# Optimization experiments

Hardware: AMD Instinct MI355X
Metric: run time of the kernel (lower is better)

Reference implementation:

```python
import jax, jax.numpy as jnp
import numpy as np

NUM_HEADS = 16
DIM_HEAD = 64
HIDDEN = 1024
CONTEXT = 200
MAX_POS = 512
INNER = NUM_HEADS * DIM_HEAD


def setup_inputs() -> dict:
    key = jax.random.key(0)
    ks = jax.random.split(key, 8)
    B, T = 8, 4000  # T is a multiple of CONTEXT (remainder == 0)
    s = 0.02
    return {
        "hidden_states": jax.random.normal(ks[0], (B, T, HIDDEN), jnp.float32),
        "ln_w": jnp.ones((HIDDEN,), jnp.float32),
        "ln_b": jnp.zeros((HIDDEN,), jnp.float32),
        "wq": jax.random.normal(ks[1], (HIDDEN, INNER), jnp.float32) * s,
        "wkv": jax.random.normal(ks[2], (HIDDEN, 2 * INNER), jnp.float32) * s,
        "wo": jax.random.normal(ks[3], (INNER, HIDDEN), jnp.float32) * s,
        "bo": jnp.zeros((HIDDEN,), jnp.float32),
        "rel_emb": jax.random.normal(ks[4], (2 * MAX_POS + 1, DIM_HEAD), jnp.float32) * s,
    }


def reference(hidden_states, ln_w, ln_b, wq, wkv, wo, bo, rel_emb):
    B, T, _ = hidden_states.shape
    nb = T // CONTEXT  # remainder == 0 by construction
    scale = DIM_HEAD ** -0.5

    # pre-norm (LayerNorm, eps=1e-5)
    mu = jnp.mean(hidden_states, axis=-1, keepdims=True)
    var = jnp.mean(jnp.square(hidden_states - mu), axis=-1, keepdims=True)
    x = (hidden_states - mu) * jax.lax.rsqrt(var + 1e-5) * ln_w + ln_b

    q = x @ wq                       # (B, T, INNER)
    kv = x @ wkv                     # (B, T, 2*INNER)
    k, v = jnp.split(kv, 2, axis=-1)

    def blk(t):  # (B, T, INNER) -> (B, nb, H, C, D)
        return t.reshape(B, nb, CONTEXT, NUM_HEADS, DIM_HEAD).transpose(0, 1, 3, 2, 4)

    q, k, v = blk(q), blk(k), blk(v)

    # Shaw relative position embeddings within a block
    seq = jnp.arange(CONTEXT)
    dist = jnp.clip(seq[:, None] - seq[None, :], -CONTEXT, CONTEXT) + MAX_POS
    rel = rel_emb[dist]              # (C, C, D)

    # pos bias: sum over head dim of q * rel  (einsum instead of broadcast-multiply-sum)
    pos_attn = jnp.einsum('bnhid,ijd->bnhij', q, rel) * scale

    # SDPA math path: softmax(q k^T * scale + bias) v
    scores = jnp.einsum('bnhid,bnhjd->bnhij', q, k) * scale + pos_attn
    attn = jax.nn.softmax(scores, axis=-1)
    out = jnp.einsum('bnhij,bnhjd->bnhid', attn, v)  # (B, nb, H, C, D)

    out = out.transpose(0, 1, 3, 2, 4).reshape(B, T, INNER)
    return out @ wo + bo  # dropout is identity in eval
```

## Files before the change

kernel.cpp:

```cpp
#include <hip/hip_runtime.h>
#include <stdint.h>
#include <stddef.h>

#define NTOK   32000
#define HID    1024
#define NQKV   3072
#define CTX    200
#define NH     16

typedef _Float16 f16;
typedef _Float16 f16x8 __attribute__((ext_vector_type(8)));
typedef _Float16 f16x4 __attribute__((ext_vector_type(4)));
typedef float    f32x4 __attribute__((ext_vector_type(4)));

__device__ __forceinline__ void async_copy16(const void* g, void* l) {
  typedef const __attribute__((address_space(1))) char gchar;
  typedef __attribute__((address_space(3))) char lchar;
  __builtin_amdgcn_global_load_lds((gchar*)g, (lchar*)l, 16, 0, 0);
}

__global__ __launch_bounds__(256) void prep_kernel(
    const float* __restrict__ wq, const float* __restrict__ wkv,
    const float* __restrict__ wo, const float* __restrict__ rel,
    f16* __restrict__ wt_qkv, f16* __restrict__ wt_o, f16* __restrict__ rel_h) {
  long idx = (long)blockIdx.x * 256 + threadIdx.x;
  if (idx < (long)NQKV * HID) {
    int n = (int)(idx >> 10), k = (int)(idx & 1023);
    float v = (n < 1024) ? wq[(size_t)k * 1024 + n] : wkv[(size_t)k * 2048 + (n - 1024)];
    wt_qkv[idx] = (f16)v;
    return;
  }
  idx -= (long)NQKV * HID;
  if (idx < (long)HID * HID) {
    int n = (int)(idx >> 10), k = (int)(idx & 1023);
    wt_o[idx] = (f16)wo[(size_t)k * 1024 + n];
    return;
  }
  idx -= (long)HID * HID;
  if (idx < 1025 * 64) rel_h[idx] = (f16)rel[idx];
}

__global__ __launch_bounds__(256) void ln_kernel(
    const float* __restrict__ hs, const float* __restrict__ lw,
    const float* __restrict__ lb, f16* __restrict__ x) {
  int tok = blockIdx.x;
  int t = threadIdx.x;
  const float4* src = (const float4*)(hs + (size_t)tok * HID);
  float4 v = src[t];
  float s  = v.x + v.y + v.z + v.w;
  float s2 = v.x * v.x + v.y * v.y + v.z * v.z + v.w * v.w;
  for (int m = 1; m < 64; m <<= 1) { s += __shfl_xor(s, m); s2 += __shfl_xor(s2, m); }
  __shared__ float ps[4], ps2[4];
  int w = t >> 6;
  if ((t & 63) == 0) { ps[w] = s; ps2[w] = s2; }
  __syncthreads();
  s  = ps[0] + ps[1] + ps[2] + ps[3];
  s2 = ps2[0] + ps2[1] + ps2[2] + ps2[3];
  float mu  = s * (1.0f / 1024.0f);
  float var = s2 * (1.0f / 1024.0f) - mu * mu;
  float rs  = rsqrtf(var + 1e-5f);
  float4 wv = ((const float4*)lw)[t];
  float4 bv = ((const float4*)lb)[t];
  f16x4 o;
  o[0] = (f16)((v.x - mu) * rs * wv.x + bv.x);
  o[1] = (f16)((v.y - mu) * rs * wv.y + bv.y);
  o[2] = (f16)((v.z - mu) * rs * wv.z + bv.z);
  o[3] = (f16)((v.w - mu) * rs * wv.w + bv.w);
  *(f16x4*)(x + (size_t)tok * HID + t * 4) = o;
}

template <int EPI>
__global__ __launch_bounds__(256) void gemm_kernel(
    const f16* __restrict__ A, const f16* __restrict__ Bt,
    void* __restrict__ C, const float* __restrict__ bias, int N) {
  __shared__ __attribute__((aligned(16))) f16 As[128 * 32];
  __shared__ __attribute__((aligned(16))) f16 Bs[128 * 32];
  int t = threadIdx.x;
  int w = t >> 6, l = t & 63;
  int m0 = blockIdx.y * 128;
  int n0 = blockIdx.x * 128;
  int wm = w >> 1, wn = w & 1;
  f32x4 acc[4][4] = {};
  int sr = t >> 2;
  int pg = t & 3;
  int lr = l & 15, lk = l >> 4;

  for (int k0 = 0; k0 < 1024; k0 += 32) {
    __syncthreads();
    #pragma unroll
    for (int c = 0; c < 2; ++c) {
      int r  = c * 64 + sr;
      int kg = pg ^ ((r >> 1) & 3);
      async_copy16(A  + (size_t)(m0 + r) * 1024 + k0 + kg * 8, (char*)As + c * 4096 + w * 1024);
      async_copy16(Bt + (size_t)(n0 + r) * 1024 + k0 + kg * 8, (char*)Bs + c * 4096 + w * 1024);
    }
    __syncthreads();
    f16x8 af[4], bf[4];
    #pragma unroll
    for (int mt = 0; mt < 4; ++mt) {
      int row = wm * 64 + mt * 16 + lr;
      int g = lk ^ ((row >> 1) & 3);
      af[mt] = *(const f16x8*)((const char*)As + row * 64 + g * 16);
    }
    #pragma unroll
    for (int nt = 0; nt < 4; ++nt) {
      int row = wn * 64 + nt * 16 + lr;
      int g = lk ^ ((row >> 1) & 3);
      bf[nt] = *(const f16x8*)((const char*)Bs + row * 64 + g * 16);
    }
    #pragma unroll
    for (int mt = 0; mt < 4; ++mt)
      #pragma unroll
      for (int nt = 0; nt < 4; ++nt)
        acc[mt][nt] = __builtin_amdgcn_mfma_f32_16x16x32_f16(af[mt], bf[nt], acc[mt][nt], 0, 0, 0);
  }

  if constexpr (EPI == 0) {
    #pragma unroll
    for (int mt = 0; mt < 4; ++mt) {
      #pragma unroll
      for (int r = 0; r < 4; ++r) {
        int grow = m0 + wm * 64 + mt * 16 + lk * 4 + r;
        unsigned bn = (unsigned)grow / 200u;
        unsigned io = (unsigned)grow - bn * 200u;
        #pragma unroll
        for (int nt = 0; nt < 4; ++nt) {
          int gcol = n0 + wn * 64 + nt * 16 + lr;
          int sel = gcol >> 10;
          int hh  = (gcol >> 6) & 15;
          int d   = gcol & 63;
          size_t addr = ((size_t)((bn * 16 + hh) * 3 + sel)) * 12800 + io * 64 + d;
          ((f16*)C)[addr] = (f16)acc[mt][nt][r];
        }
      }
    }
  } else {
    #pragma unroll
    for (int mt = 0; mt < 4; ++mt)
      #pragma unroll
      for (int nt = 0; nt < 4; ++nt) {
        int gcol = n0 + wn * 64 + nt * 16 + lr;
        #pragma unroll
        for (int r = 0; r < 4; ++r) {
          int grow = m0 + wm * 64 + mt * 16 + lk * 4 + r;
          ((float*)C)[(size_t)grow * N + gcol] = acc[mt][nt][r] + bias[gcol];
        }
      }
  }
}

__global__ __launch_bounds__(256, 2) void attn_kernel(
    const f16* __restrict__ qkvb, const f16* __restrict__ rel_h,
    f16* __restrict__ out) {
  __shared__ __attribute__((aligned(16))) f16 Ks[208 * 64];
  __shared__ __attribute__((aligned(16))) f16 Vt[64 * 200];
  __shared__ __attribute__((aligned(16))) f16 Gb[4][215 * 17];

  int bh = blockIdx.x;
  int h  = bh & 15;
  size_t t0 = (size_t)(bh >> 4) * CTX;
  int t = threadIdx.x;
  int w = t >> 6, l = t & 63;
  int lr = l & 15, lk = l >> 4;

  const f16* Qb = qkvb + (size_t)bh * 38400;
  const f16* Kb = Qb + 12800;
  const f16* Vb = Qb + 25600;

  for (int it = w; it < 26; it += 4) {
    int srow = it * 8 + (l >> 3);
    int pg   = l & 7;
    int grow = srow < 200 ? srow : 199;
    int gg   = pg ^ (srow & 7);
    async_copy16(Kb + (size_t)grow * 64 + gg * 8, (char*)Ks + it * 1024);
  }
  {
    const f16* vcol = Vb + l;
    for (int g = w; g < 50; g += 4) {
      int j = g * 4;
      f16x4 pk;
      #pragma unroll
      for (int u = 0; u < 4; ++u) pk[u] = vcol[(size_t)(j + u) * 64];
      *(f16x4*)(Vt + l * 200 + j) = pk;
    }
  }
  __syncthreads();

  f16* gb = Gb[w];

  for (int c = w; c < 13; c += 4) {
    int m0 = c * 16;
    int qrow = m0 + lr; if (qrow > 199) qrow = 199;
    f16x8 bq0 = *(const f16x8*)(Qb + (size_t)qrow * 64 + lk * 8);
    f16x8 bq1 = *(const f16x8*)(Qb + (size_t)qrow * 64 + 32 + lk * 8);
    bq0 = bq0 * (f16)0.125f;
    bq1 = bq1 * (f16)0.125f;

    f32x4 S[13];
    #pragma unroll
    for (int ts = 0; ts < 13; ++ts) {
      int row = ts * 16 + lr;
      int sw  = row & 7;
      f16x8 a0 = *(const f16x8*)(Ks + row * 64 + (lk ^ sw) * 8);
      f16x8 a1 = *(const f16x8*)(Ks + row * 64 + ((4 + lk) ^ sw) * 8);
      f32x4 a = {};
      a = __builtin_amdgcn_mfma_f32_16x16x32_f16(a0, bq0, a, 0, 0, 0);
      S[ts] = __builtin_amdgcn_mfma_f32_16x16x32_f16(a1, bq1, a, 0, 0, 0);
    }

    const f16* rb = rel_h + (size_t)(313 + m0) * 64;
    #pragma unroll
    for (int tg = 0; tg < 14; ++tg) {
      int pr = tg * 16 + lr;
      f16x8 a0 = *(const f16x8*)(rb + (size_t)pr * 64 + lk * 8);
      f16x8 a1 = *(const f16x8*)(rb + (size_t)pr * 64 + 32 + lk * 8);
      f32x4 g = {};
      g = __builtin_amdgcn_mfma_f32_16x16x32_f16(a0, bq0, g, 0, 0, 0);
      g = __builtin_amdgcn_mfma_f32_16x16x32_f16(a1, bq1, g, 0, 0, 0);
      #pragma unroll
      for (int r = 0; r < 4; ++r) {
        int pp2 = tg * 16 + 4 * lk + r;
        if (pp2 <= 214) gb[pp2 * 17 + lr] = (f16)g[r];
      }
    }

    #pragma unroll
    for (int ts = 0; ts < 13; ++ts) {
      #pragma unroll
      for (int r = 0; r < 4; ++r) {
        int pp = lr + 199 - ts * 16 - 4 * lk - r;
        if (pp < 0) pp = 0;
        S[ts][r] += (float)gb[pp * 17 + lr];
      }
    }
    #pragma unroll
    for (int r = 0; r < 4; ++r)
      if (4 * lk + r >= 8) S[12][r] = -1e30f;

    float mx = -1e30f;
    #pragma unroll
    for (int ts = 0; ts < 13; ++ts)
      #pragma unroll
      for (int r = 0; r < 4; ++r) mx = fmaxf(mx, S[ts][r]);
    mx = fmaxf(mx, __shfl_xor(mx, 16));
    mx = fmaxf(mx, __shfl_xor(mx, 32));
    float sum = 0.f;
    #pragma unroll
    for (int ts = 0; ts < 13; ++ts)
      #pragma unroll
      for (int r = 0; r < 4; ++r) {
        float e = __expf(S[ts][r] - mx);
        S[ts][r] = e;
        sum += e;
      }
    sum += __shfl_xor(sum, 16);
    sum += __shfl_xor(sum, 32);
    float inv = 1.0f / sum;

    f16x4 P[13];
    #pragma unroll
    for (int ts = 0; ts < 13; ++ts)
      #pragma unroll
      for (int r = 0; r < 4; ++r) P[ts][r] = (f16)(S[ts][r] * inv);

    f32x4 o[4] = {};
    #pragma unroll
    for (int ts = 0; ts < 13; ++ts) {
      int col4 = ts * 16 + 4 * lk;
      if (col4 > 196) col4 = 196;
      #pragma unroll
      for (int dt = 0; dt < 4; ++dt) {
        f16x4 bv = *(const f16x4*)(Vt + (dt * 16 + lr) * 200 + col4);
        o[dt] = __builtin_amdgcn_mfma_f32_16x16x16f16(P[ts], bv, o[dt], 0, 0, 0);
      }
    }

    {
      f16* ob = gb;
      #pragma unroll
      for (int dt = 0; dt < 4; ++dt)
        #pragma unroll
        for (int r = 0; r < 4; ++r)
          ob[(4 * lk + r) * 72 + dt * 16 + lr] = (f16)o[dt][r];
      int orow = l >> 2;
      int ocol = (l & 3) * 16;
      if (m0 + orow < 200) {
        f16x8 v0 = *(const f16x8*)(ob + orow * 72 + ocol);
        f16x8 v1 = *(const f16x8*)(ob + orow * 72 + ocol + 8);
        f16* dst = out + (t0 + m0 + orow) * HID + h * 64 + ocol;
        *(f16x8*)dst = v0;
        *(f16x8*)(dst + 8) = v1;
      }
    }
  }
}

extern "C" void kernel_launch(void* const* d_in, const int* in_sizes, int n_in,
                              void* d_out, int out_size, void* d_ws, size_t ws_size,
                              hipStream_t stream) {
  const float* hs  = (const float*)d_in[0];
  const float* lnw = (const float*)d_in[1];
  const float* lnb = (const float*)d_in[2];
  const float* wq  = (const float*)d_in[3];
  const float* wkv = (const float*)d_in[4];
  const float* wo  = (const float*)d_in[5];
  const float* bo  = (const float*)d_in[6];
  const float* rel = (const float*)d_in[7];

  char* ws = (char*)d_ws;
  f16* x     = (f16*)(ws);
  f16* qkvb  = (f16*)(ws + 65536000);
  f16* wtqkv = (f16*)(ws + 65536000 + 196608000);
  f16* wto   = (f16*)(ws + 65536000 + 196608000 + 6291456);
  f16* rel_h = (f16*)(ws + 65536000 + 196608000 + 6291456 + 2097152);
  f16* attn  = x;

  {
    long total = (long)NQKV * HID + (long)HID * HID + 1025 * 64;
    int grid = (int)((total + 255) / 256);
    prep_kernel<<<grid, 256, 0, stream>>>(wq, wkv, wo, rel, wtqkv, wto, rel_h);
  }
  ln_kernel<<<NTOK, 256, 0, stream>>>(hs, lnw, lnb, x);
  gemm_kernel<0><<<dim3(NQKV / 128, NTOK / 128), 256, 0, stream>>>(x, wtqkv, (void*)qkvb, nullptr, NQKV);
  attn_kernel<<<2560, 256, 0, stream>>>(qkvb, rel_h, attn);
  gemm_kernel<1><<<dim3(HID / 128, NTOK / 128), 256, 0, stream>>>(attn, wto, d_out, bo, HID);
}
```

Measured before the change: 761.6 us.

## Rewrite GEMM as 256x256 tile, 8-wave kernel with double-buffered async pipeline

Replaces the 128x128, 4-wave GEMM with a 256x256 tile, 512-thread kernel. It double-buffers K=64 slices in 128KB of LDS with XOR swizzling and interleaves async global-to-LDS copies with MFMA quarters, using explicit waitcnt, barriers and setprio. It also remaps workgroups so each XCD gets contiguous tiles for better L2 locality. The intent is more reuse per loaded byte and hiding load latency behind compute. The costs are higher register and LDS pressure, which limits occupancy, and more fragile hand-tuned synchronisation.

```diff
diff --git a/kernel.cpp b/kernel.cpp
--- a/kernel.cpp
+++ b/kernel.cpp
@@ -70,80 +70,144 @@
 }
 
 template <int EPI>
-__global__ __launch_bounds__(256) void gemm_kernel(
+__global__ __launch_bounds__(512, 2) void gemm_kernel(
     const f16* __restrict__ A, const f16* __restrict__ Bt,
     void* __restrict__ C, const float* __restrict__ bias, int N) {
-  __shared__ __attribute__((aligned(16))) f16 As[128 * 32];
-  __shared__ __attribute__((aligned(16))) f16 Bs[128 * 32];
+  __shared__ __attribute__((aligned(16))) f16 sm[4][16384];
+
   int t = threadIdx.x;
   int w = t >> 6, l = t & 63;
-  int m0 = blockIdx.y * 128;
-  int n0 = blockIdx.x * 128;
-  int wm = w >> 1, wn = w & 1;
-  f32x4 acc[4][4] = {};
-  int sr = t >> 2;
-  int pg = t & 3;
+  int wm = w >> 2, wn = w & 3;
   int lr = l & 15, lk = l >> 4;
-
-  for (int k0 = 0; k0 < 1024; k0 += 32) {
-    __syncthreads();
-    #pragma unroll
-    for (int c = 0; c < 2; ++c) {
-      int r  = c * 64 + sr;
-      int kg = pg ^ ((r >> 1) & 3);
-      async_copy16(A  + (size_t)(m0 + r) * 1024 + k0 + kg * 8, (char*)As + c * 4096 + w * 1024);
-      async_copy16(Bt + (size_t)(n0 + r) * 1024 + k0 + kg * 8, (char*)Bs + c * 4096 + w * 1024);
-    }
-    __syncthreads();
-    f16x8 af[4], bf[4];
-    #pragma unroll
-    for (int mt = 0; mt < 4; ++mt) {
-      int row = wm * 64 + mt * 16 + lr;
-      int g = lk ^ ((row >> 1) & 3);
-      af[mt] = *(const f16x8*)((const char*)As + row * 64 + g * 16);
-    }
-    #pragma unroll
-    for (int nt = 0; nt < 4; ++nt) {
-      int row = wn * 64 + nt * 16 + lr;
-      int g = lk ^ ((row >> 1) & 3);
-      bf[nt] = *(const f16x8*)((const char*)Bs + row * 64 + g * 16);
-    }
-    #pragma unroll
-    for (int mt = 0; mt < 4; ++mt)
-      #pragma unroll
-      for (int nt = 0; nt < 4; ++nt)
-        acc[mt][nt] = __builtin_amdgcn_mfma_f32_16x16x32_f16(af[mt], bf[nt], acc[mt][nt], 0, 0, 0);
-  }
+  int sw = lr & 7;
+  const int sg_off = ((l >> 3) << 10) + (((l & 7) ^ (l >> 3)) << 3);
+
+  int nwg = (int)(gridDim.x * gridDim.y);
+  int lid = (int)(blockIdx.y * gridDim.x + blockIdx.x);
+  int q = nwg >> 3, r = nwg & 7;
+  int xcd = lid & 7, loc = lid >> 3;
+  int nid = (xcd < r ? xcd * (q + 1) : r * (q + 1) + (xcd - r) * q) + loc;
+  int bx = nid % (int)gridDim.x, by = nid / (int)gridDim.x;
+  const int m0 = by * 256, n0 = bx * 256;
+
+  f32x4 acc[8][4] = {};
+  f16x8 a[8], b[8];
+
+#define STG(reg, half, gsrc, row0, kt) do {                                        \
+    const f16* _s = (gsrc) + (size_t)((row0) + (half) * 128 + w * 16) * 1024       \
+                    + (kt) * 64 + sg_off;                                          \
+    char* _d = (char*)(reg) + (half) * 16384 + w * 2048;                           \
+    async_copy16(_s, _d);                                                          \
+    async_copy16(_s + 8 * 1024, _d + 1024);                                        \
+  } while (0)
+
+#define LDA(As_, Mh) do {                                                          \
+    _Pragma("unroll") for (int mt = 0; mt < 4; ++mt) {                             \
+      int row_ = wm * 128 + (Mh) * 64 + mt * 16 + lr;                              \
+      _Pragma("unroll") for (int ks = 0; ks < 2; ++ks)                             \
+        a[mt * 2 + ks] = *(const f16x8*)((As_) + row_ * 64                         \
+                          + (((ks * 4 + lk) ^ sw) << 3));                          \
+    } } while (0)
+
+#define LDB(Bs_, Nh) do {                                                          \
+    _Pragma("unroll") for (int nt = 0; nt < 2; ++nt) {                             \
+      int row_ = wn * 64 + (Nh) * 32 + nt * 16 + lr;                               \
+      _Pragma("unroll") for (int ks = 0; ks < 2; ++ks)                             \
+        b[(Nh) * 4 + nt * 2 + ks] = *(const f16x8*)((Bs_) + row_ * 64              \
+                          + (((ks * 4 + lk) ^ sw) << 3));                          \
+    } } while (0)
+
+#define MMA(Mh, Nh) do {                                                           \
+    __builtin_amdgcn_s_setprio(1);                                                 \
+    _Pragma("unroll") for (int mt = 0; mt < 4; ++mt)                               \
+    _Pragma("unroll") for (int nt = 0; nt < 2; ++nt)                               \
+    _Pragma("unroll") for (int ks = 0; ks < 2; ++ks)                               \
+      acc[(Mh) * 4 + mt][(Nh) * 2 + nt] = __builtin_amdgcn_mfma_f32_16x16x32_f16(  \
+          a[mt * 2 + ks], b[(Nh) * 4 + nt * 2 + ks],                               \
+          acc[(Mh) * 4 + mt][(Nh) * 2 + nt], 0, 0, 0);                             \
+    __builtin_amdgcn_s_setprio(0); } while (0)
+
+#define BAR  __builtin_amdgcn_s_barrier()
+#define WLG  asm volatile("s_waitcnt lgkmcnt(0)" ::: "memory")
+#define WVM6 asm volatile("s_waitcnt vmcnt(6)" ::: "memory")
+
+  STG(sm[1], 0, Bt, n0, 0);
+  STG(sm[1], 1, Bt, n0, 0);
+  STG(sm[0], 0, A, m0, 0);
+  STG(sm[0], 1, A, m0, 0);
+  asm volatile("s_waitcnt vmcnt(4)" ::: "memory");
+  STG(sm[3], 0, Bt, n0, 1);
+  STG(sm[3], 1, Bt, n0, 1);
+  STG(sm[2], 0, A, m0, 1);
+  WVM6;
+  BAR;
+
+  for (int j = 0; j < 8; ++j) {
+    int k1 = 2 * j + 1;
+    int ke = (2 * j + 2 > 14) ? 14 : 2 * j + 2;
+    int ko = (2 * j + 3 > 15) ? 15 : 2 * j + 3;
+    LDA(sm[0], 0); LDB(sm[1], 0);
+    STG(sm[2], 1, A, m0, k1);
+    BAR; WLG; MMA(0, 0); BAR;
+    LDB(sm[1], 1);
+    STG(sm[1], 0, Bt, n0, ke);
+    BAR; WLG; MMA(0, 1); BAR;
+    LDA(sm[0], 1);
+    STG(sm[1], 1, Bt, n0, ke);
+    BAR; WLG; MMA(1, 0); BAR;
+    STG(sm[0], 0, A, m0, ke);
+    BAR; MMA(1, 1); WVM6; BAR;
+    LDA(sm[2], 0); LDB(sm[3], 0);
+    STG(sm[0], 1, A, m0, ke);
+    BAR; WLG; MMA(0, 0); BAR;
+    LDB(sm[3], 1);
+    STG(sm[3], 0, Bt, n0, ko);
+    BAR; WLG; MMA(0, 1); BAR;
+    LDA(sm[2], 1);
+    STG(sm[3], 1, Bt, n0, ko);
+    BAR; WLG; MMA(1, 0); BAR;
+    STG(sm[2], 0, A, m0, ko);
+    BAR; MMA(1, 1); WVM6; BAR;
+  }
+
+#undef STG
+#undef LDA
+#undef LDB
+#undef MMA
+#undef BAR
+#undef WLG
+#undef WVM6
 
   if constexpr (EPI == 0) {
     #pragma unroll
-    for (int mt = 0; mt < 4; ++mt) {
-      #pragma unroll
-      for (int r = 0; r < 4; ++r) {
-        int grow = m0 + wm * 64 + mt * 16 + lk * 4 + r;
+    for (int mt = 0; mt < 8; ++mt) {
+      #pragma unroll
+      for (int rr = 0; rr < 4; ++rr) {
+        int grow = m0 + wm * 128 + mt * 16 + lk * 4 + rr;
         unsigned bn = (unsigned)grow / 200u;
         unsigned io = (unsigned)grow - bn * 200u;
+        size_t rowb = (size_t)bn * 614400 + (size_t)io * 64;
         #pragma unroll
         for (int nt = 0; nt < 4; ++nt) {
           int gcol = n0 + wn * 64 + nt * 16 + lr;
           int sel = gcol >> 10;
           int hh  = (gcol >> 6) & 15;
           int d   = gcol & 63;
-          size_t addr = ((size_t)((bn * 16 + hh) * 3 + sel)) * 12800 + io * 64 + d;
-          ((f16*)C)[addr] = (f16)acc[mt][nt][r];
+          ((f16*)C)[rowb + (size_t)(hh * 3 + sel) * 12800 + d] = (f16)acc[mt][nt][rr];
         }
       }
     }
   } else {
     #pragma unroll
-    for (int mt = 0; mt < 4; ++mt)
+    for (int mt = 0; mt < 8; ++mt)
       #pragma unroll
       for (int nt = 0; nt < 4; ++nt) {
         int gcol = n0 + wn * 64 + nt * 16 + lr;
+        float bv = bias[gcol];
         #pragma unroll
-        for (int r = 0; r < 4; ++r) {
-          int grow = m0 + wm * 64 + mt * 16 + lk * 4 + r;
-          ((float*)C)[(size_t)grow * N + gcol] = acc[mt][nt][r] + bias[gcol];
+        for (int rr = 0; rr < 4; ++rr) {
+          int grow = m0 + wm * 128 + mt * 16 + lk * 4 + rr;
+          ((float*)C)[(size_t)grow * N + gcol] = acc[mt][nt][rr] + bv;
         }
       }
   }
@@ -321,7 +385,7 @@
     prep_kernel<<<grid, 256, 0, stream>>>(wq, wkv, wo, rel, wtqkv, wto, rel_h);
   }
   ln_kernel<<<NTOK, 256, 0, stream>>>(hs, lnw, lnb, x);
-  gemm_kernel<0><<<dim3(NQKV / 128, NTOK / 128), 256, 0, stream>>>(x, wtqkv, (void*)qkvb, nullptr, NQKV);
+  gemm_kernel<0><<<dim3(NQKV / 256, NTOK / 256), 512, 0, stream>>>(x, wtqkv, (void*)qkvb, nullptr, NQKV);
   attn_kernel<<<2560, 256, 0, stream>>>(qkvb, rel_h, attn);
-  gemm_kernel<1><<<dim3(HID / 128, NTOK / 128), 256, 0, stream>>>(attn, wto, d_out, bo, HID);
-}
+  gemm_kernel<1><<<dim3(HID / 256, NTOK / 256), 512, 0, stream>>>(attn, wto, d_out, bo, HID);
+}
```

New measurement: 682.9 us. 10.3% less time.
